# Kernel tuning notes

Hardware: AMD Instinct MI355X
Metric: run time of the kernel (lower is better)

The kernel has to match this reference:

```python
import jax, jax.numpy as jnp
import numpy as np

B, N, H, NH = 2, 2048, 1024, 16
D = H // NH  # head_dim = 64


def setup_inputs() -> dict:
    key = jax.random.key(0)
    ks = jax.random.split(key, 12)
    s = 0.02
    inp = {
        'q': jax.random.normal(ks[0], (B, N, H), jnp.float32),
        'k': jax.random.normal(ks[1], (B, N, H), jnp.float32),
        'v': jax.random.normal(ks[2], (B, N, H), jnp.float32),
        # causal mask: 1 where attending allowed, 0 above diagonal
        'mask': jnp.tril(jnp.ones((N, N), jnp.float32))[None, None],
        'Wq': jax.random.normal(ks[3], (H, H), jnp.float32) * s,
        'bq': jnp.zeros((H,), jnp.float32),
        'Wk': jax.random.normal(ks[4], (H, H), jnp.float32) * s,
        'bk': jnp.zeros((H,), jnp.float32),
        'Wv': jax.random.normal(ks[5], (H, H), jnp.float32) * s,
        'bv': jnp.zeros((H,), jnp.float32),
        'Wp': jax.random.normal(ks[6], (H, H), jnp.float32) * s,
        'bp': jnp.zeros((H,), jnp.float32),
    }
    return inp


def _split_heads(x):
    # [b, n, (h d)] -> [b, h, n, d]
    b, n, _ = x.shape
    return x.reshape(b, n, NH, D).transpose(0, 2, 1, 3)


def reference(q, k, v, mask, Wq, bq, Wk, bk, Wv, bv, Wp, bp):
    # torch nn.Linear: x @ W.T + b
    Q = _split_heads(q @ Wq.T + bq)                      # [b, h, n, d]
    K = _split_heads(k @ Wk.T + bk)
    V = _split_heads(v @ Wv.T + bv)
    scores = jnp.einsum('bhnd,bhmd->bhnm', Q, K) / jnp.sqrt(jnp.float32(D))
    scores = jnp.where(mask == 0, -jnp.inf, scores)      # masked_fill
    attn = jax.nn.softmax(scores, axis=-1)
    out = jnp.einsum('bhnm,bhmd->bhnd', attn, V)         # [b, h, n, d]
    out = out.transpose(0, 2, 1, 3).reshape(q.shape[0], q.shape[1], H)
    # dropout is identity in eval mode
    return out @ Wp.T + bp
```

## Files before the change

kernel.cpp:

```cpp
#include <hip/hip_runtime.h>

typedef unsigned short u16;
typedef __attribute__((ext_vector_type(8))) short bf16x8;
typedef __attribute__((ext_vector_type(4))) short bf16x4;
typedef __attribute__((ext_vector_type(4))) float f32x4;

#define NB 2
#define SEQ 2048
#define HID 1024
#define NHEAD 16
#define HD 64
#define MROWS (NB * SEQ)

__device__ __forceinline__ float bf2f(u16 u) {
  union { unsigned u; float f; } x; x.u = ((unsigned)u) << 16; return x.f;
}
__device__ __forceinline__ u16 f2bf(float f) {
  union { float f; unsigned u; } x; x.f = f;
  unsigned r = x.u + 0x7fffu + ((x.u >> 16) & 1u);
  return (u16)(r >> 16);
}
__device__ __forceinline__ u16 f2bf_trunc(float f) {
  union { float f; unsigned u; } x; x.f = f;
  return (u16)(x.u >> 16);
}

#define GLOAD_LDS16(g, l)                                                   \
  __builtin_amdgcn_global_load_lds(                                         \
      (const __attribute__((address_space(1))) void*)(g),                   \
      (__attribute__((address_space(3))) void*)(l), 16, 0, 0)

__global__ __launch_bounds__(256)
void conv_all(const float* __restrict__ q, const float* __restrict__ k,
              const float* __restrict__ v, const float* __restrict__ wq,
              const float* __restrict__ wk, const float* __restrict__ wv,
              const float* __restrict__ wp, u16* __restrict__ qb,
              u16* __restrict__ kb, u16* __restrict__ vb,
              u16* __restrict__ wcat, u16* __restrict__ wpb)
{
  const int i = blockIdx.x * 256 + threadIdx.x;
  const float* s; u16* d;
  if (i < 1572864) {
    const int seg = i / 524288;
    const int off = i - seg * 524288;
    s = (seg == 0 ? q : seg == 1 ? k : v) + (size_t)off * 8;
    d = (seg == 0 ? qb : seg == 1 ? kb : vb) + (size_t)off * 8;
  } else {
    const int j = i - 1572864;
    const int seg = j / 131072;
    const int off = j - seg * 131072;
    s = (seg == 0 ? wq : seg == 1 ? wk : seg == 2 ? wv : wp) + (size_t)off * 8;
    d = (seg < 3 ? wcat + (size_t)seg * 1048576 : wpb) + (size_t)off * 8;
  }
  f32x4 a = *(const f32x4*)s;
  f32x4 b = *(const f32x4*)(s + 4);
  bf16x8 o;
#pragma unroll
  for (int j = 0; j < 4; ++j) { o[j] = (short)f2bf(a[j]); o[4 + j] = (short)f2bf(b[j]); }
  *(bf16x8*)d = o;
}

__global__ __launch_bounds__(256)
void gemm_qkv(const u16* __restrict__ A0, const u16* __restrict__ A1,
              const u16* __restrict__ A2, const u16* __restrict__ Wcat,
              const float* __restrict__ b0, const float* __restrict__ b1,
              const float* __restrict__ b2,
              u16* __restrict__ Qh, u16* __restrict__ Kh, u16* __restrict__ Vt,
              float qscale)
{
  __shared__ u16 As[2 * 128 * 64];
  __shared__ u16 Bs[2 * 128 * 64];
  const int p = blockIdx.x;
  const int c = p & 7;
  const int i_ = p >> 3;
  const int G = c * 12 + (i_ % 12);
  const int j = i_ / 12;
  const int g = G >> 5;
  const int m0 = (G & 31) * 128;
  const int n0 = (g * 8 + j) * 128;
  const u16* A = (g == 0) ? A0 : (g == 1) ? A1 : A2;
  const float* bias = (g == 0) ? b0 : (g == 1) ? b1 : b2;
  const int t = threadIdx.x, lane = t & 63, w = t >> 6;
  const int grp = lane >> 4, lr = lane & 15;
  const int wr = (w >> 1) * 64, wc = (w & 1) * 64;
  const int sw8 = lr & 7;

  f32x4 acc[4][4];
#pragma unroll
  for (int i = 0; i < 4; ++i)
#pragma unroll
    for (int j2 = 0; j2 < 4; ++j2) acc[i][j2] = (f32x4){0.f, 0.f, 0.f, 0.f};

  const int srow8 = lane >> 3;
  const int achunk = ((lane & 7) ^ srow8) * 8;
  const u16* ag = A + (size_t)(m0 + w * 32 + srow8) * HID + achunk;
  const u16* wg = Wcat + (size_t)(n0 + w * 32 + srow8) * HID + achunk;

#define STAGE(BI, K0)                                                \
  {                                                                  \
    const u16* ab = ag + (K0);                                       \
    const u16* wb = wg + (K0);                                       \
    u16* al = As + (BI) * 8192 + (w * 32) * 64;                      \
    u16* bl = Bs + (BI) * 8192 + (w * 32) * 64;                      \
    GLOAD_LDS16(ab, al);                                             \
    GLOAD_LDS16(ab + (size_t)8 * HID, al + 8 * 64);                  \
    GLOAD_LDS16(ab + (size_t)16 * HID, al + 16 * 64);                \
    GLOAD_LDS16(ab + (size_t)24 * HID, al + 24 * 64);                \
    GLOAD_LDS16(wb, bl);                                             \
    GLOAD_LDS16(wb + (size_t)8 * HID, bl + 8 * 64);                  \
    GLOAD_LDS16(wb + (size_t)16 * HID, bl + 16 * 64);                \
    GLOAD_LDS16(wb + (size_t)24 * HID, bl + 24 * 64);                \
  }

  STAGE(0, 0);

  for (int it = 0; it < 16; ++it) {
    const int cur = it & 1;
    asm volatile("s_waitcnt vmcnt(0)" ::: "memory");
    __builtin_amdgcn_s_barrier();
    __builtin_amdgcn_sched_barrier(0);
    asm volatile("" ::: "memory");
    if (it < 15) STAGE(cur ^ 1, (it + 1) * 64);
    const u16* Ab = As + cur * 8192;
    const u16* Bb = Bs + cur * 8192;
#pragma unroll
    for (int kh = 0; kh < 2; ++kh) {
      bf16x8 af[4], bf[4];
#pragma unroll
      for (int mi = 0; mi < 4; ++mi)
        af[mi] = *(const bf16x8*)&Ab[(wr + mi * 16 + lr) * 64 +
                                     (((kh * 4 + grp) ^ sw8) * 8)];
#pragma unroll
      for (int ni = 0; ni < 4; ++ni)
        bf[ni] = *(const bf16x8*)&Bb[(wc + ni * 16 + lr) * 64 +
                                     (((kh * 4 + grp) ^ sw8) * 8)];
      __builtin_amdgcn_s_setprio(1);
#pragma unroll
      for (int mi = 0; mi < 4; ++mi)
#pragma unroll
        for (int ni = 0; ni < 4; ++ni)
          acc[mi][ni] = __builtin_amdgcn_mfma_f32_16x16x32_bf16(
              af[mi], bf[ni], acc[mi][ni], 0, 0, 0);
      __builtin_amdgcn_s_setprio(0);
    }
  }
#undef STAGE

  const float scale = (g == 0) ? qscale : 1.f;
#pragma unroll
  for (int mi = 0; mi < 4; ++mi) {
#pragma unroll
    for (int ni = 0; ni < 4; ++ni) {
      const int nl = (n0 & (HID - 1)) + wc + ni * 16 + lr;
      const float bval = bias[nl];
      const int mb = m0 + wr + mi * 16 + grp * 4;
      const int h = nl >> 6, d = nl & (HD - 1);
      if (g == 2) {
        const int b = mb >> 11, nn = mb & (SEQ - 1);
        bf16x4 pk;
#pragma unroll
        for (int r = 0; r < 4; ++r)
          pk[r] = (short)f2bf(acc[mi][ni][r] + bval);
        *(bf16x4*)&Vt[((size_t)(b * NHEAD + h) * HD + d) * SEQ + nn] = pk;
      } else {
        u16* O = (g == 0) ? Qh : Kh;
#pragma unroll
        for (int r = 0; r < 4; ++r) {
          const int m = mb + r;
          const int b = m >> 11, nn = m & (SEQ - 1);
          O[((size_t)(b * NHEAD + h) * SEQ + nn) * HD + d] =
              f2bf((acc[mi][ni][r] + bval) * scale);
        }
      }
    }
  }
}

__global__ __launch_bounds__(256)
void gemm_proj(const u16* __restrict__ A, const u16* __restrict__ W,
               const float* __restrict__ bias, float* __restrict__ Op)
{
  __shared__ u16 As[2 * 128 * 64];
  __shared__ u16 Bs[2 * 128 * 64];
  const int p = blockIdx.x;
  const int c = p & 7;
  const int i_ = p >> 3;
  const int G = c * 4 + (i_ & 3);
  const int j = i_ >> 2;
  const int m0 = G * 128, n0 = j * 128;
  const int t = threadIdx.x, lane = t & 63, w = t >> 6;
  const int grp = lane >> 4, lr = lane & 15;
  const int wr = (w >> 1) * 64, wc = (w & 1) * 64;
  const int sw8 = lr & 7;

  f32x4 acc[4][4];
#pragma unroll
  for (int i = 0; i < 4; ++i)
#pragma unroll
    for (int j2 = 0; j2 < 4; ++j2) acc[i][j2] = (f32x4){0.f, 0.f, 0.f, 0.f};

  const int srow8 = lane >> 3;
  const int achunk = ((lane & 7) ^ srow8) * 8;
  const u16* ag = A + (size_t)(m0 + w * 32 + srow8) * HID + achunk;
  const u16* wg = W + (size_t)(n0 + w * 32 + srow8) * HID + achunk;

#define STAGE(BI, K0)                                                \
  {                                                                  \
    const u16* ab = ag + (K0);                                       \
    const u16* wb = wg + (K0);                                       \
    u16* al = As + (BI) * 8192 + (w * 32) * 64;                      \
    u16* bl = Bs + (BI) * 8192 + (w * 32) * 64;                      \
    GLOAD_LDS16(ab, al);                                             \
    GLOAD_LDS16(ab + (size_t)8 * HID, al + 8 * 64);                  \
    GLOAD_LDS16(ab + (size_t)16 * HID, al + 16 * 64);                \
    GLOAD_LDS16(ab + (size_t)24 * HID, al + 24 * 64);                \
    GLOAD_LDS16(wb, bl);                                             \
    GLOAD_LDS16(wb + (size_t)8 * HID, bl + 8 * 64);                  \
    GLOAD_LDS16(wb + (size_t)16 * HID, bl + 16 * 64);                \
    GLOAD_LDS16(wb + (size_t)24 * HID, bl + 24 * 64);                \
  }

  STAGE(0, 0);

  for (int it = 0; it < 16; ++it) {
    const int cur = it & 1;
    asm volatile("s_waitcnt vmcnt(0)" ::: "memory");
    __builtin_amdgcn_s_barrier();
    __builtin_amdgcn_sched_barrier(0);
    asm volatile("" ::: "memory");
    if (it < 15) STAGE(cur ^ 1, (it + 1) * 64);
    const u16* Ab = As + cur * 8192;
    const u16* Bb = Bs + cur * 8192;
#pragma unroll
    for (int kh = 0; kh < 2; ++kh) {
      bf16x8 af[4], bf[4];
#pragma unroll
      for (int mi = 0; mi < 4; ++mi)
        af[mi] = *(const bf16x8*)&Ab[(wr + mi * 16 + lr) * 64 +
                                     (((kh * 4 + grp) ^ sw8) * 8)];
#pragma unroll
      for (int ni = 0; ni < 4; ++ni)
        bf[ni] = *(const bf16x8*)&Bb[(wc + ni * 16 + lr) * 64 +
                                     (((kh * 4 + grp) ^ sw8) * 8)];
      __builtin_amdgcn_s_setprio(1);
#pragma unroll
      for (int mi = 0; mi < 4; ++mi)
#pragma unroll
        for (int ni = 0; ni < 4; ++ni)
          acc[mi][ni] = __builtin_amdgcn_mfma_f32_16x16x32_bf16(
              af[mi], bf[ni], acc[mi][ni], 0, 0, 0);
      __builtin_amdgcn_s_setprio(0);
    }
  }
#undef STAGE

#pragma unroll
  for (int mi = 0; mi < 4; ++mi) {
#pragma unroll
    for (int ni = 0; ni < 4; ++ni) {
      const int n = n0 + wc + ni * 16 + lr;
      const float bval = bias[n];
      const int mb = m0 + wr + mi * 16 + grp * 4;
#pragma unroll
      for (int r = 0; r < 4; ++r)
        Op[(size_t)(mb + r) * HID + n] = acc[mi][ni][r] + bval;
    }
  }
}

__global__ __launch_bounds__(512)
void attn_fwd(const u16* __restrict__ Q, const u16* __restrict__ K,
              const u16* __restrict__ Vt, u16* __restrict__ parO,
              float* __restrict__ parL)
{
  __shared__ u16 KB[2][4096];
  __shared__ u16 VB[2][4096];
  const int bh = blockIdx.y;
  const int t = threadIdx.x;
  const int w = t >> 6, lane = t & 63;
  const int grp = lane >> 4, lr = lane & 15;
  const int px = blockIdx.x;
  const int parity = px & 1;
  const int qtA = px >> 1;
  const int qtB = 15 - qtA;
  const int q0A = qtA * 128 + w * 16;
  const int q0B = qtB * 128 + w * 16;
  const int ntB = 2 * qtB + 2;
  const size_t base = (size_t)bh * SEQ * HD;
  const float NEGINF = -__builtin_inff();

  const int srow = lane >> 3;
  const int scol = (lane & 7) ^ srow;
  const u16* kg = K + base + (size_t)(w * 8 + srow) * HD + scol * 8;
  const u16* vg = Vt + base + (size_t)(w * 8 + srow) * SEQ + scol * 8;

  const bf16x8 aqA0 = *(const bf16x8*)&Q[base + (size_t)(q0A + lr) * HD + grp * 8];
  const bf16x8 aqA1 = *(const bf16x8*)&Q[base + (size_t)(q0A + lr) * HD + grp * 8 + 32];
  const bf16x8 aqB0 = *(const bf16x8*)&Q[base + (size_t)(q0B + lr) * HD + grp * 8];
  const bf16x8 aqB1 = *(const bf16x8*)&Q[base + (size_t)(q0B + lr) * HD + grp * 8 + 32];

  float lA = 0.f, lB = 0.f;
  f32x4 oA[4], oB[4];
#pragma unroll
  for (int c = 0; c < 4; ++c) {
    oA[c] = (f32x4){0.f, 0.f, 0.f, 0.f};
    oB[c] = (f32x4){0.f, 0.f, 0.f, 0.f};
  }

  const int idqA = q0A >> 6;
  const int idqB = q0B >> 6;
  const int sw = lr & 7;

#define STAGE(bi, j0)                                              \
  {                                                                \
    GLOAD_LDS16(kg + (size_t)(j0) * HD, &KB[bi][w * 512]);         \
    GLOAD_LDS16(vg + (j0), &VB[bi][w * 512]);                      \
  }

#define COMPUTE(Q0, AQ0, AQ1, OACC, LI, IDQ)                                  \
  do {                                                                        \
    f32x4 sv[4];                                                              \
    __builtin_amdgcn_s_setprio(1);                                            \
    _Pragma("unroll")                                                         \
    for (int st = 0; st < 4; ++st) {                                          \
      const int ro = (st * 16 + lr) * 64;                                     \
      bf16x8 k0 = *(const bf16x8*)&KB[bi][ro + ((grp ^ sw) * 8)];             \
      bf16x8 k1 = *(const bf16x8*)&KB[bi][ro + (((grp + 4) ^ sw) * 8)];       \
      f32x4 s = (f32x4){0.f, 0.f, 0.f, 0.f};                                  \
      s = __builtin_amdgcn_mfma_f32_16x16x32_bf16(k0, (AQ0), s, 0, 0, 0);     \
      s = __builtin_amdgcn_mfma_f32_16x16x32_bf16(k1, (AQ1), s, 0, 0, 0);     \
      sv[st] = s;                                                             \
    }                                                                         \
    __builtin_amdgcn_s_setprio(0);                                            \
    bf16x4 bv[4][4];                                                          \
    _Pragma("unroll")                                                         \
    for (int st = 0; st < 4; ++st)                                            \
      _Pragma("unroll")                                                       \
      for (int c = 0; c < 4; ++c)                                             \
        bv[st][c] = *(const bf16x4*)&VB[bi][(c * 16 + lr) * 64 +              \
                        (((st * 2 + (grp >> 1)) ^ sw) * 8) + (grp & 1) * 4];  \
    if (it == (IDQ)) {                                                        \
      const int j0 = it << 6, qg = (Q0) + lr;                                 \
      _Pragma("unroll")                                                       \
      for (int st = 0; st < 4; ++st)                                          \
        _Pragma("unroll")                                                     \
        for (int r = 0; r < 4; ++r)                                           \
          if (j0 + st * 16 + grp * 4 + r > qg) sv[st][r] = NEGINF;            \
    }                                                                         \
    float rs = 0.f;                                                           \
    _Pragma("unroll")                                                         \
    for (int st = 0; st < 4; ++st)                                            \
      _Pragma("unroll")                                                       \
      for (int r = 0; r < 4; ++r) {                                           \
        sv[st][r] = exp2f(sv[st][r]);                                         \
        rs += sv[st][r];                                                      \
      }                                                                       \
    (LI) += rs;                                                               \
    bf16x4 pa[4];                                                             \
    _Pragma("unroll")                                                         \
    for (int st = 0; st < 4; ++st)                                            \
      _Pragma("unroll")                                                       \
      for (int r = 0; r < 4; ++r) pa[st][r] = (short)f2bf_trunc(sv[st][r]);   \
    __builtin_amdgcn_s_setprio(1);                                            \
    _Pragma("unroll")                                                         \
    for (int st = 0; st < 4; ++st)                                            \
      _Pragma("unroll")                                                       \
      for (int c = 0; c < 4; ++c)                                             \
        (OACC)[c] = __builtin_amdgcn_mfma_f32_16x16x16bf16_1k(                \
            pa[st], bv[st][c], (OACC)[c], 0, 0, 0);                           \
    __builtin_amdgcn_s_setprio(0);                                            \
  } while (0)

  STAGE(0, parity << 6);

  for (int it = parity; it < ntB; it += 2) {
    const int bi = ((it - parity) >> 1) & 1;
    asm volatile("s_waitcnt vmcnt(0)" ::: "memory");
    __builtin_amdgcn_s_barrier();
    __builtin_amdgcn_sched_barrier(0);
    asm volatile("" ::: "memory");
    if (it + 2 < ntB) STAGE(bi ^ 1, (it + 2) << 6);

    if (it <= idqB) COMPUTE(q0B, aqB0, aqB1, oB, lB, idqB);
    if (it <= idqA) COMPUTE(q0A, aqA0, aqA1, oA, lA, idqA);
  }
#undef STAGE
#undef COMPUTE

  lB += __shfl_xor(lB, 16);  lB += __shfl_xor(lB, 32);
  lA += __shfl_xor(lA, 16);  lA += __shfl_xor(lA, 32);

  const size_t pbase = (size_t)(parity * 32 + bh) * SEQ;
  if (grp == 0) {
    parL[pbase + q0B + lr] = lB;
    parL[pbase + q0A + lr] = lA;
  }
#pragma unroll
  for (int r = 0; r < 4; ++r) {
    const int nB = q0B + grp * 4 + r;
    const int nA = q0A + grp * 4 + r;
#pragma unroll
    for (int c = 0; c < 4; ++c) {
      parO[(pbase + nB) * HD + c * 16 + lr] = f2bf(oB[c][r]);
      parO[(pbase + nA) * HD + c * 16 + lr] = f2bf(oA[c][r]);
    }
  }
}

__global__ __launch_bounds__(256)
void combine(const u16* __restrict__ parO, const float* __restrict__ parL,
             u16* __restrict__ AO)
{
  const int i = blockIdx.x * 256 + threadIdx.x;
  const int bh = i >> 14;
  const int rem = i & 16383;
  const int n = rem >> 3;
  const int d0 = (rem & 7) * 8;
  const size_t q0 = (size_t)bh * SEQ + n;
  const float inv = 1.f / (parL[q0] + parL[q0 + 65536]);
  const u16* p0 = parO + q0 * HD + d0;
  const u16* p1 = p0 + (size_t)4194304;
  bf16x8 a = *(const bf16x8*)p0;
  bf16x8 b = *(const bf16x8*)p1;
  bf16x8 o;
#pragma unroll
  for (int j = 0; j < 8; ++j)
    o[j] = (short)f2bf((bf2f((u16)a[j]) + bf2f((u16)b[j])) * inv);
  const int bb = bh >> 4, h = bh & 15;
  *(bf16x8*)&AO[((size_t)(bb * SEQ + n)) * HID + h * HD + d0] = o;
}

extern "C" void kernel_launch(void* const* d_in, const int* in_sizes, int n_in,
                              void* d_out, int out_size, void* d_ws, size_t ws_size,
                              hipStream_t stream) {
  const float* q  = (const float*)d_in[0];
  const float* k  = (const float*)d_in[1];
  const float* v  = (const float*)d_in[2];
  const float* Wq = (const float*)d_in[4];
  const float* bq = (const float*)d_in[5];
  const float* Wk = (const float*)d_in[6];
  const float* bk = (const float*)d_in[7];
  const float* Wv = (const float*)d_in[8];
  const float* bv = (const float*)d_in[9];
  const float* Wp = (const float*)d_in[10];
  const float* bp = (const float*)d_in[11];
  float* out = (float*)d_out;

  char* ws = (char*)d_ws;
  u16*   qb   = (u16*)(ws);
  u16*   kb   = (u16*)(ws + ( 8u << 20));
  u16*   vb   = (u16*)(ws + (16u << 20));
  u16*   Wcat = (u16*)(ws + (24u << 20));
  u16*   Wpb  = (u16*)(ws + (30u << 20));
  u16*   Qh   = (u16*)(ws + (32u << 20));
  u16*   Kh   = (u16*)(ws + (40u << 20));
  u16*   Vt   = (u16*)(ws + (48u << 20));
  u16*   parO = (u16*)(ws);
  float* parL = (float*)(ws + (17u << 20));
  u16*   AO   = (u16*)(ws + (18u << 20));

  const float qscale = 0.125f * 1.4426950408889634f;

  conv_all<<<8192, 256, 0, stream>>>(q, k, v, Wq, Wk, Wv, Wp,
                                     qb, kb, vb, Wcat, Wpb);
  gemm_qkv<<<768, 256, 0, stream>>>(
      qb, kb, vb, Wcat, bq, bk, bv, Qh, Kh, Vt, qscale);
  attn_fwd<<<dim3(16, NB * NHEAD), 512, 0, stream>>>(Qh, Kh, Vt, parO, parL);
  combine<<<2048, 256, 0, stream>>>(parO, parL, AO);
  gemm_proj<<<256, 256, 0, stream>>>(AO, Wpb, bp, out);
}
```

Measured before the change: 123.6 us.

## Fuse input bf16 conversion into QKV GEMM and split-combine into projection GEMM

The QKV GEMM now loads fp32 activations directly, converts them to bf16 in registers and writes them into swizzled LDS, so the separate activation conversion pass and its bf16 round trip through memory go away. The projection GEMM likewise reads the two partial attention outputs and their normalisers, combines them on the fly and stages the result into LDS, which removes the combine kernel and the AO buffer. Both GEMMs move to 128x64 tiles with twice as many blocks to keep parallelism up. The cost is that every N-tile block rereads and reconverts the same A rows (fp32 for QKV, two bf16 partials for projection), and the register-staged A path adds conversion work and manual vmcnt pipelining inside the main loop.

```diff
diff --git a/kernel.cpp b/kernel.cpp
--- a/kernel.cpp
+++ b/kernel.cpp
@@ -31,27 +31,16 @@
       (__attribute__((address_space(3))) void*)(l), 16, 0, 0)
 
 __global__ __launch_bounds__(256)
-void conv_all(const float* __restrict__ q, const float* __restrict__ k,
-              const float* __restrict__ v, const float* __restrict__ wq,
-              const float* __restrict__ wk, const float* __restrict__ wv,
-              const float* __restrict__ wp, u16* __restrict__ qb,
-              u16* __restrict__ kb, u16* __restrict__ vb,
-              u16* __restrict__ wcat, u16* __restrict__ wpb)
+void conv_w(const float* __restrict__ wq, const float* __restrict__ wk,
+            const float* __restrict__ wv, const float* __restrict__ wp,
+            u16* __restrict__ wcat, u16* __restrict__ wpb)
 {
   const int i = blockIdx.x * 256 + threadIdx.x;
-  const float* s; u16* d;
-  if (i < 1572864) {
-    const int seg = i / 524288;
-    const int off = i - seg * 524288;
-    s = (seg == 0 ? q : seg == 1 ? k : v) + (size_t)off * 8;
-    d = (seg == 0 ? qb : seg == 1 ? kb : vb) + (size_t)off * 8;
-  } else {
-    const int j = i - 1572864;
-    const int seg = j / 131072;
-    const int off = j - seg * 131072;
-    s = (seg == 0 ? wq : seg == 1 ? wk : seg == 2 ? wv : wp) + (size_t)off * 8;
-    d = (seg < 3 ? wcat + (size_t)seg * 1048576 : wpb) + (size_t)off * 8;
-  }
+  const int seg = i >> 17;
+  const int off = i & 131071;
+  const float* s = (seg == 0 ? wq : seg == 1 ? wk : seg == 2 ? wv : wp) +
+                   (size_t)off * 8;
+  u16* d = (seg < 3 ? wcat + (size_t)seg * 1048576 : wpb) + (size_t)off * 8;
   f32x4 a = *(const f32x4*)s;
   f32x4 b = *(const f32x4*)(s + 4);
   bf16x8 o;
@@ -61,97 +50,119 @@
 }
 
 __global__ __launch_bounds__(256)
-void gemm_qkv(const u16* __restrict__ A0, const u16* __restrict__ A1,
-              const u16* __restrict__ A2, const u16* __restrict__ Wcat,
+void gemm_qkv(const float* __restrict__ A0, const float* __restrict__ A1,
+              const float* __restrict__ A2, const u16* __restrict__ Wcat,
               const float* __restrict__ b0, const float* __restrict__ b1,
               const float* __restrict__ b2,
               u16* __restrict__ Qh, u16* __restrict__ Kh, u16* __restrict__ Vt,
               float qscale)
 {
   __shared__ u16 As[2 * 128 * 64];
-  __shared__ u16 Bs[2 * 128 * 64];
+  __shared__ u16 Bs[2 * 64 * 64];
   const int p = blockIdx.x;
-  const int c = p & 7;
+  const int cx = p & 7;
   const int i_ = p >> 3;
-  const int G = c * 12 + (i_ % 12);
-  const int j = i_ / 12;
+  const int G = cx * 12 + (i_ >> 4);
+  const int j = i_ & 15;
   const int g = G >> 5;
   const int m0 = (G & 31) * 128;
-  const int n0 = (g * 8 + j) * 128;
-  const u16* A = (g == 0) ? A0 : (g == 1) ? A1 : A2;
+  const int nloc0 = j * 64;
+  const float* A = (g == 0) ? A0 : (g == 1) ? A1 : A2;
   const float* bias = (g == 0) ? b0 : (g == 1) ? b1 : b2;
   const int t = threadIdx.x, lane = t & 63, w = t >> 6;
   const int grp = lane >> 4, lr = lane & 15;
-  const int wr = (w >> 1) * 64, wc = (w & 1) * 64;
+  const int wr = (w >> 1) * 64, wc = (w & 1) * 32;
   const int sw8 = lr & 7;
 
-  f32x4 acc[4][4];
+  f32x4 acc[4][2];
 #pragma unroll
   for (int i = 0; i < 4; ++i)
 #pragma unroll
-    for (int j2 = 0; j2 < 4; ++j2) acc[i][j2] = (f32x4){0.f, 0.f, 0.f, 0.f};
+    for (int j2 = 0; j2 < 2; ++j2) acc[i][j2] = (f32x4){0.f, 0.f, 0.f, 0.f};
 
   const int srow8 = lane >> 3;
   const int achunk = ((lane & 7) ^ srow8) * 8;
-  const u16* ag = A + (size_t)(m0 + w * 32 + srow8) * HID + achunk;
-  const u16* wg = Wcat + (size_t)(n0 + w * 32 + srow8) * HID + achunk;
-
-#define STAGE(BI, K0)                                                \
-  {                                                                  \
-    const u16* ab = ag + (K0);                                       \
-    const u16* wb = wg + (K0);                                       \
-    u16* al = As + (BI) * 8192 + (w * 32) * 64;                      \
-    u16* bl = Bs + (BI) * 8192 + (w * 32) * 64;                      \
-    GLOAD_LDS16(ab, al);                                             \
-    GLOAD_LDS16(ab + (size_t)8 * HID, al + 8 * 64);                  \
-    GLOAD_LDS16(ab + (size_t)16 * HID, al + 16 * 64);                \
-    GLOAD_LDS16(ab + (size_t)24 * HID, al + 24 * 64);                \
-    GLOAD_LDS16(wb, bl);                                             \
-    GLOAD_LDS16(wb + (size_t)8 * HID, bl + 8 * 64);                  \
-    GLOAD_LDS16(wb + (size_t)16 * HID, bl + 16 * 64);                \
-    GLOAD_LDS16(wb + (size_t)24 * HID, bl + 24 * 64);                \
-  }
-
-  STAGE(0, 0);
+  const u16* wg = Wcat + (size_t)(g * 1024 + nloc0 + w * 16 + srow8) * HID + achunk;
+  const int r = t >> 1, kh2 = t & 1;
+  const float* ag = A + (size_t)(m0 + r) * HID + kh2 * 32;
+  const int wbase = r * 64 + 0;
+
+  f32x4 a4[8];
+#define ALOADQ(K0)                                                    \
+  { const float* pp = ag + (K0);                                      \
+    a4[0] = *(const f32x4*)(pp);      a4[1] = *(const f32x4*)(pp + 4);  \
+    a4[2] = *(const f32x4*)(pp + 8);  a4[3] = *(const f32x4*)(pp + 12); \
+    a4[4] = *(const f32x4*)(pp + 16); a4[5] = *(const f32x4*)(pp + 20); \
+    a4[6] = *(const f32x4*)(pp + 24); a4[7] = *(const f32x4*)(pp + 28); }
+#define ACONVQ(BI)                                                    \
+  { _Pragma("unroll")                                                 \
+    for (int jj = 0; jj < 4; ++jj) {                                  \
+      bf16x8 o;                                                       \
+      _Pragma("unroll")                                               \
+      for (int e = 0; e < 4; ++e) {                                   \
+        o[e]     = (short)f2bf(a4[2 * jj][e]);                        \
+        o[4 + e] = (short)f2bf(a4[2 * jj + 1][e]);                    \
+      }                                                               \
+      const int q = kh2 * 4 + jj;                                     \
+      *(bf16x8*)&As[(BI) * 8192 + wbase + ((q ^ (r & 7)) * 8)] = o;   \
+    } }
+#define WSTAGEQ(BI, K0)                                               \
+  { const u16* wb = wg + (K0);                                        \
+    u16* bl = Bs + (BI) * 4096 + (w * 16) * 64;                       \
+    GLOAD_LDS16(wb, bl);                                              \
+    GLOAD_LDS16(wb + (size_t)8 * HID, bl + 8 * 64); }
+
+  ALOADQ(0);
+  asm volatile("s_waitcnt vmcnt(0)" ::: "memory");
+  ACONVQ(0);
+  WSTAGEQ(0, 0);
+  ALOADQ(64);
+  asm volatile("s_waitcnt lgkmcnt(0)" ::: "memory");
 
   for (int it = 0; it < 16; ++it) {
     const int cur = it & 1;
-    asm volatile("s_waitcnt vmcnt(0)" ::: "memory");
+    asm volatile("s_waitcnt vmcnt(8)" ::: "memory");
     __builtin_amdgcn_s_barrier();
     __builtin_amdgcn_sched_barrier(0);
     asm volatile("" ::: "memory");
-    if (it < 15) STAGE(cur ^ 1, (it + 1) * 64);
+    WSTAGEQ(cur ^ 1, (it + 1 < 16) ? (it + 1) * 64 : 0);
     const u16* Ab = As + cur * 8192;
-    const u16* Bb = Bs + cur * 8192;
+    const u16* Bb = Bs + cur * 4096;
 #pragma unroll
     for (int kh = 0; kh < 2; ++kh) {
-      bf16x8 af[4], bf[4];
+      bf16x8 af[4], bf[2];
 #pragma unroll
       for (int mi = 0; mi < 4; ++mi)
         af[mi] = *(const bf16x8*)&Ab[(wr + mi * 16 + lr) * 64 +
                                      (((kh * 4 + grp) ^ sw8) * 8)];
 #pragma unroll
-      for (int ni = 0; ni < 4; ++ni)
+      for (int ni = 0; ni < 2; ++ni)
         bf[ni] = *(const bf16x8*)&Bb[(wc + ni * 16 + lr) * 64 +
                                      (((kh * 4 + grp) ^ sw8) * 8)];
       __builtin_amdgcn_s_setprio(1);
 #pragma unroll
       for (int mi = 0; mi < 4; ++mi)
 #pragma unroll
-        for (int ni = 0; ni < 4; ++ni)
+        for (int ni = 0; ni < 2; ++ni)
           acc[mi][ni] = __builtin_amdgcn_mfma_f32_16x16x32_bf16(
               af[mi], bf[ni], acc[mi][ni], 0, 0, 0);
       __builtin_amdgcn_s_setprio(0);
     }
-  }
-#undef STAGE
+    asm volatile("s_waitcnt vmcnt(2)" ::: "memory");
+    ACONVQ(cur ^ 1);
+    ALOADQ((it + 2 < 16) ? (it + 2) * 64 : 0);
+    asm volatile("s_waitcnt lgkmcnt(0)" ::: "memory");
+  }
+#undef ALOADQ
+#undef ACONVQ
+#undef WSTAGEQ
 
   const float scale = (g == 0) ? qscale : 1.f;
 #pragma unroll
   for (int mi = 0; mi < 4; ++mi) {
 #pragma unroll
-    for (int ni = 0; ni < 4; ++ni) {
-      const int nl = (n0 & (HID - 1)) + wc + ni * 16 + lr;
+    for (int ni = 0; ni < 2; ++ni) {
+      const int nl = nloc0 + wc + ni * 16 + lr;
       const float bval = bias[nl];
       const int mb = m0 + wr + mi * 16 + grp * 4;
       const int h = nl >> 6, d = nl & (HD - 1);
@@ -159,17 +170,17 @@
         const int b = mb >> 11, nn = mb & (SEQ - 1);
         bf16x4 pk;
 #pragma unroll
-        for (int r = 0; r < 4; ++r)
-          pk[r] = (short)f2bf(acc[mi][ni][r] + bval);
+        for (int rr = 0; rr < 4; ++rr)
+          pk[rr] = (short)f2bf(acc[mi][ni][rr] + bval);
         *(bf16x4*)&Vt[((size_t)(b * NHEAD + h) * HD + d) * SEQ + nn] = pk;
       } else {
         u16* O = (g == 0) ? Qh : Kh;
 #pragma unroll
-        for (int r = 0; r < 4; ++r) {
-          const int m = mb + r;
+        for (int rr = 0; rr < 4; ++rr) {
+          const int m = mb + rr;
           const int b = m >> 11, nn = m & (SEQ - 1);
           O[((size_t)(b * NHEAD + h) * SEQ + nn) * HD + d] =
-              f2bf((acc[mi][ni][r] + bval) * scale);
+              f2bf((acc[mi][ni][rr] + bval) * scale);
         }
       }
     }
@@ -177,93 +188,124 @@
 }
 
 __global__ __launch_bounds__(256)
-void gemm_proj(const u16* __restrict__ A, const u16* __restrict__ W,
-               const float* __restrict__ bias, float* __restrict__ Op)
+void gemm_proj(const u16* __restrict__ parO, const float* __restrict__ parL,
+               const u16* __restrict__ W, const float* __restrict__ bias,
+               float* __restrict__ Op)
 {
   __shared__ u16 As[2 * 128 * 64];
-  __shared__ u16 Bs[2 * 128 * 64];
+  __shared__ u16 Bs[2 * 64 * 64];
   const int p = blockIdx.x;
-  const int c = p & 7;
+  const int cx = p & 7;
   const int i_ = p >> 3;
-  const int G = c * 4 + (i_ & 3);
+  const int G = cx * 4 + (i_ & 3);
   const int j = i_ >> 2;
-  const int m0 = G * 128, n0 = j * 128;
+  const int m0 = G * 128, n0 = j * 64;
   const int t = threadIdx.x, lane = t & 63, w = t >> 6;
   const int grp = lane >> 4, lr = lane & 15;
-  const int wr = (w >> 1) * 64, wc = (w & 1) * 64;
+  const int wr = (w >> 1) * 64, wc = (w & 1) * 32;
   const int sw8 = lr & 7;
 
-  f32x4 acc[4][4];
+  f32x4 acc[4][2];
 #pragma unroll
   for (int i = 0; i < 4; ++i)
 #pragma unroll
-    for (int j2 = 0; j2 < 4; ++j2) acc[i][j2] = (f32x4){0.f, 0.f, 0.f, 0.f};
+    for (int j2 = 0; j2 < 2; ++j2) acc[i][j2] = (f32x4){0.f, 0.f, 0.f, 0.f};
 
   const int srow8 = lane >> 3;
   const int achunk = ((lane & 7) ^ srow8) * 8;
-  const u16* ag = A + (size_t)(m0 + w * 32 + srow8) * HID + achunk;
-  const u16* wg = W + (size_t)(n0 + w * 32 + srow8) * HID + achunk;
-
-#define STAGE(BI, K0)                                                \
-  {                                                                  \
-    const u16* ab = ag + (K0);                                       \
-    const u16* wb = wg + (K0);                                       \
-    u16* al = As + (BI) * 8192 + (w * 32) * 64;                      \
-    u16* bl = Bs + (BI) * 8192 + (w * 32) * 64;                      \
-    GLOAD_LDS16(ab, al);                                             \
-    GLOAD_LDS16(ab + (size_t)8 * HID, al + 8 * 64);                  \
-    GLOAD_LDS16(ab + (size_t)16 * HID, al + 16 * 64);                \
-    GLOAD_LDS16(ab + (size_t)24 * HID, al + 24 * 64);                \
-    GLOAD_LDS16(wb, bl);                                             \
-    GLOAD_LDS16(wb + (size_t)8 * HID, bl + 8 * 64);                  \
-    GLOAD_LDS16(wb + (size_t)16 * HID, bl + 16 * 64);                \
-    GLOAD_LDS16(wb + (size_t)24 * HID, bl + 24 * 64);                \
-  }
-
-  STAGE(0, 0);
+  const u16* wg = W + (size_t)(n0 + w * 16 + srow8) * HID + achunk;
+  const int r = t >> 1, dh = t & 1;
+  const int m = m0 + r;
+  const int b = m >> 11, nn = m & (SEQ - 1);
+  const u16* po0 = parO + ((size_t)(b * NHEAD) * SEQ + nn) * HD + dh * 32;
+  const u16* po1 = po0 + (size_t)32 * SEQ * HD;
+  const float* pl0 = parL + (size_t)(b * NHEAD) * SEQ + nn;
+  const int wbase = r * 64;
+
+  bf16x8 av[8];
+  float l0, l1;
+#define ALOADP(H)                                                     \
+  { const u16* q0 = po0 + (size_t)(H) * (SEQ * HD);                   \
+    const u16* q1 = po1 + (size_t)(H) * (SEQ * HD);                   \
+    av[0] = *(const bf16x8*)(q0);      av[1] = *(const bf16x8*)(q0 + 8);  \
+    av[2] = *(const bf16x8*)(q0 + 16); av[3] = *(const bf16x8*)(q0 + 24); \
+    av[4] = *(const bf16x8*)(q1);      av[5] = *(const bf16x8*)(q1 + 8);  \
+    av[6] = *(const bf16x8*)(q1 + 16); av[7] = *(const bf16x8*)(q1 + 24); \
+    l0 = pl0[(size_t)(H) * SEQ];                                      \
+    l1 = pl0[(size_t)(H) * SEQ + 32 * SEQ]; }
+#define ACONVP(BI)                                                    \
+  { const float inv = 1.f / (l0 + l1);                                \
+    _Pragma("unroll")                                                 \
+    for (int jj = 0; jj < 4; ++jj) {                                  \
+      bf16x8 o;                                                       \
+      _Pragma("unroll")                                               \
+      for (int e = 0; e < 8; ++e)                                     \
+        o[e] = (short)f2bf((bf2f((u16)av[jj][e]) +                    \
+                            bf2f((u16)av[4 + jj][e])) * inv);         \
+      const int q = dh * 4 + jj;                                      \
+      *(bf16x8*)&As[(BI) * 8192 + wbase + ((q ^ (r & 7)) * 8)] = o;   \
+    } }
+#define WSTAGEP(BI, K0)                                               \
+  { const u16* wb = wg + (K0);                                        \
+    u16* bl = Bs + (BI) * 4096 + (w * 16) * 64;                       \
+    GLOAD_LDS16(wb, bl);                                              \
+    GLOAD_LDS16(wb + (size_t)8 * HID, bl + 8 * 64); }
+
+  ALOADP(0);
+  asm volatile("s_waitcnt vmcnt(0)" ::: "memory");
+  ACONVP(0);
+  WSTAGEP(0, 0);
+  ALOADP(1);
+  asm volatile("s_waitcnt lgkmcnt(0)" ::: "memory");
 
   for (int it = 0; it < 16; ++it) {
     const int cur = it & 1;
-    asm volatile("s_waitcnt vmcnt(0)" ::: "memory");
+    asm volatile("s_waitcnt vmcnt(10)" ::: "memory");
     __builtin_amdgcn_s_barrier();
     __builtin_amdgcn_sched_barrier(0);
     asm volatile("" ::: "memory");
-    if (it < 15) STAGE(cur ^ 1, (it + 1) * 64);
+    WSTAGEP(cur ^ 1, (it + 1 < 16) ? (it + 1) * 64 : 0);
     const u16* Ab = As + cur * 8192;
-    const u16* Bb = Bs + cur * 8192;
+    const u16* Bb = Bs + cur * 4096;
 #pragma unroll
     for (int kh = 0; kh < 2; ++kh) {
-      bf16x8 af[4], bf[4];
+      bf16x8 af[4], bf[2];
 #pragma unroll
       for (int mi = 0; mi < 4; ++mi)
         af[mi] = *(const bf16x8*)&Ab[(wr + mi * 16 + lr) * 64 +
                                      (((kh * 4 + grp) ^ sw8) * 8)];
 #pragma unroll
-      for (int ni = 0; ni < 4; ++ni)
+      for (int ni = 0; ni < 2; ++ni)
         bf[ni] = *(const bf16x8*)&Bb[(wc + ni * 16 + lr) * 64 +
                                      (((kh * 4 + grp) ^ sw8) * 8)];
       __builtin_amdgcn_s_setprio(1);
 #pragma unroll
       for (int mi = 0; mi < 4; ++mi)
 #pragma unroll
-        for (int ni = 0; ni < 4; ++ni)
+        for (int ni = 0; ni < 2; ++ni)
           acc[mi][ni] = __builtin_amdgcn_mfma_f32_16x16x32_bf16(
               af[mi], bf[ni], acc[mi][ni], 0, 0, 0);
       __builtin_amdgcn_s_setprio(0);
     }
-  }
-#undef STAGE
+    asm volatile("s_waitcnt vmcnt(2)" ::: "memory");
+    ACONVP(cur ^ 1);
+    ALOADP((it + 2 < 16) ? (it + 2) : 0);
+    asm volatile("s_waitcnt lgkmcnt(0)" ::: "memory");
+  }
+#undef ALOADP
+#undef ACONVP
+#undef WSTAGEP
 
 #pragma unroll
   for (int mi = 0; mi < 4; ++mi) {
 #pragma unroll
-    for (int ni = 0; ni < 4; ++ni) {
+    for (int ni = 0; ni < 2; ++ni) {
       const int n = n0 + wc + ni * 16 + lr;
       const float bval = bias[n];
       const int mb = m0 + wr + mi * 16 + grp * 4;
 #pragma unroll
-      for (int r = 0; r < 4; ++r)
-        Op[(size_t)(mb + r) * HID + n] = acc[mi][ni][r] + bval;
+      for (int rr = 0; rr < 4; ++rr)
+        Op[(size_t)(mb + rr) * HID + n] = acc[mi][ni][rr] + bval;
     }
   }
 }
@@ -407,29 +449,6 @@
   }
 }
 
-__global__ __launch_bounds__(256)
-void combine(const u16* __restrict__ parO, const float* __restrict__ parL,
-             u16* __restrict__ AO)
-{
-  const int i = blockIdx.x * 256 + threadIdx.x;
-  const int bh = i >> 14;
-  const int rem = i & 16383;
-  const int n = rem >> 3;
-  const int d0 = (rem & 7) * 8;
-  const size_t q0 = (size_t)bh * SEQ + n;
-  const float inv = 1.f / (parL[q0] + parL[q0 + 65536]);
-  const u16* p0 = parO + q0 * HD + d0;
-  const u16* p1 = p0 + (size_t)4194304;
-  bf16x8 a = *(const bf16x8*)p0;
-  bf16x8 b = *(const bf16x8*)p1;
-  bf16x8 o;
-#pragma unroll
-  for (int j = 0; j < 8; ++j)
-    o[j] = (short)f2bf((bf2f((u16)a[j]) + bf2f((u16)b[j])) * inv);
-  const int bb = bh >> 4, h = bh & 15;
-  *(bf16x8*)&AO[((size_t)(bb * SEQ + n)) * HID + h * HD + d0] = o;
-}
-
 extern "C" void kernel_launch(void* const* d_in, const int* in_sizes, int n_in,
                               void* d_out, int out_size, void* d_ws, size_t ws_size,
                               hipStream_t stream) {
@@ -447,25 +466,19 @@
   float* out = (float*)d_out;
 
   char* ws = (char*)d_ws;
-  u16*   qb   = (u16*)(ws);
-  u16*   kb   = (u16*)(ws + ( 8u << 20));
-  u16*   vb   = (u16*)(ws + (16u << 20));
+  u16*   parO = (u16*)(ws);
+  float* parL = (float*)(ws + (17u << 20));
   u16*   Wcat = (u16*)(ws + (24u << 20));
   u16*   Wpb  = (u16*)(ws + (30u << 20));
   u16*   Qh   = (u16*)(ws + (32u << 20));
   u16*   Kh   = (u16*)(ws + (40u << 20));
   u16*   Vt   = (u16*)(ws + (48u << 20));
-  u16*   parO = (u16*)(ws);
-  float* parL = (float*)(ws + (17u << 20));
-  u16*   AO   = (u16*)(ws + (18u << 20));
 
   const float qscale = 0.125f * 1.4426950408889634f;
 
-  conv_all<<<8192, 256, 0, stream>>>(q, k, v, Wq, Wk, Wv, Wp,
-                                     qb, kb, vb, Wcat, Wpb);
-  gemm_qkv<<<768, 256, 0, stream>>>(
-      qb, kb, vb, Wcat, bq, bk, bv, Qh, Kh, Vt, qscale);
+  conv_w<<<2048, 256, 0, stream>>>(Wq, Wk, Wv, Wp, Wcat, Wpb);
+  gemm_qkv<<<1536, 256, 0, stream>>>(
+      q, k, v, Wcat, bq, bk, bv, Qh, Kh, Vt, qscale);
   attn_fwd<<<dim3(16, NB * NHEAD), 512, 0, stream>>>(Qh, Kh, Vt, parO, parL);
-  combine<<<2048, 256, 0, stream>>>(parO, parL, AO);
-  gemm_proj<<<256, 256, 0, stream>>>(AO, Wpb, bp, out);
-}
+  gemm_proj<<<512, 256, 0, stream>>>(parO, parL, Wpb, bp, out);
+}
```

Result: slower. 183.9 us (+48.8%).

## Fuse split-KV combine into output projection GEMM A-operand staging

Applied to the files above, without the earlier changes.

Removes the separate combine kernel by having gemm_proj read the two partial attention outputs and their row sums directly, normalise them in registers, and write the bf16 A tile into LDS. The N tile is halved to 64 so the grid doubles to 512 blocks, giving better CU fill. A-operand loads now go through registers with manual vmcnt bookkeeping instead of direct-to-LDS loads. The cost is that each partial output is re-read and re-normalised once per N tile (16 times instead of once), and the correctness of the pipelining depends on hand-counted waitcnt values.

```diff
diff --git a/kernel.cpp b/kernel.cpp
--- a/kernel.cpp
+++ b/kernel.cpp
@@ -177,93 +177,124 @@
 }
 
 __global__ __launch_bounds__(256)
-void gemm_proj(const u16* __restrict__ A, const u16* __restrict__ W,
-               const float* __restrict__ bias, float* __restrict__ Op)
+void gemm_proj(const u16* __restrict__ parO, const float* __restrict__ parL,
+               const u16* __restrict__ W, const float* __restrict__ bias,
+               float* __restrict__ Op)
 {
   __shared__ u16 As[2 * 128 * 64];
-  __shared__ u16 Bs[2 * 128 * 64];
+  __shared__ u16 Bs[2 * 64 * 64];
   const int p = blockIdx.x;
-  const int c = p & 7;
+  const int cx = p & 7;
   const int i_ = p >> 3;
-  const int G = c * 4 + (i_ & 3);
+  const int G = cx * 4 + (i_ & 3);
   const int j = i_ >> 2;
-  const int m0 = G * 128, n0 = j * 128;
+  const int m0 = G * 128, n0 = j * 64;
   const int t = threadIdx.x, lane = t & 63, w = t >> 6;
   const int grp = lane >> 4, lr = lane & 15;
-  const int wr = (w >> 1) * 64, wc = (w & 1) * 64;
+  const int wr = (w >> 1) * 64, wc = (w & 1) * 32;
   const int sw8 = lr & 7;
 
-  f32x4 acc[4][4];
+  f32x4 acc[4][2];
 #pragma unroll
   for (int i = 0; i < 4; ++i)
 #pragma unroll
-    for (int j2 = 0; j2 < 4; ++j2) acc[i][j2] = (f32x4){0.f, 0.f, 0.f, 0.f};
+    for (int j2 = 0; j2 < 2; ++j2) acc[i][j2] = (f32x4){0.f, 0.f, 0.f, 0.f};
 
   const int srow8 = lane >> 3;
   const int achunk = ((lane & 7) ^ srow8) * 8;
-  const u16* ag = A + (size_t)(m0 + w * 32 + srow8) * HID + achunk;
-  const u16* wg = W + (size_t)(n0 + w * 32 + srow8) * HID + achunk;
-
-#define STAGE(BI, K0)                                                \
-  {                                                                  \
-    const u16* ab = ag + (K0);                                       \
-    const u16* wb = wg + (K0);                                       \
-    u16* al = As + (BI) * 8192 + (w * 32) * 64;                      \
-    u16* bl = Bs + (BI) * 8192 + (w * 32) * 64;                      \
-    GLOAD_LDS16(ab, al);                                             \
-    GLOAD_LDS16(ab + (size_t)8 * HID, al + 8 * 64);                  \
-    GLOAD_LDS16(ab + (size_t)16 * HID, al + 16 * 64);                \
-    GLOAD_LDS16(ab + (size_t)24 * HID, al + 24 * 64);                \
-    GLOAD_LDS16(wb, bl);                                             \
-    GLOAD_LDS16(wb + (size_t)8 * HID, bl + 8 * 64);                  \
-    GLOAD_LDS16(wb + (size_t)16 * HID, bl + 16 * 64);                \
-    GLOAD_LDS16(wb + (size_t)24 * HID, bl + 24 * 64);                \
-  }
-
-  STAGE(0, 0);
+  const u16* wg = W + (size_t)(n0 + w * 16 + srow8) * HID + achunk;
+  const int r = t >> 1, dh = t & 1;
+  const int m = m0 + r;
+  const int b = m >> 11, nn = m & (SEQ - 1);
+  const u16* po0 = parO + ((size_t)(b * NHEAD) * SEQ + nn) * HD + dh * 32;
+  const u16* po1 = po0 + (size_t)32 * SEQ * HD;
+  const float* pl0 = parL + (size_t)(b * NHEAD) * SEQ + nn;
+  const int wbase = r * 64;
+
+  bf16x8 av[8];
+  float l0, l1;
+#define ALOADP(H)                                                     \
+  { const u16* q0 = po0 + (size_t)(H) * (SEQ * HD);                   \
+    const u16* q1 = po1 + (size_t)(H) * (SEQ * HD);                   \
+    av[0] = *(const bf16x8*)(q0);      av[1] = *(const bf16x8*)(q0 + 8);  \
+    av[2] = *(const bf16x8*)(q0 + 16); av[3] = *(const bf16x8*)(q0 + 24); \
+    av[4] = *(const bf16x8*)(q1);      av[5] = *(const bf16x8*)(q1 + 8);  \
+    av[6] = *(const bf16x8*)(q1 + 16); av[7] = *(const bf16x8*)(q1 + 24); \
+    l0 = pl0[(size_t)(H) * SEQ];                                      \
+    l1 = pl0[(size_t)(H) * SEQ + 32 * SEQ]; }
+#define ACONVP(BI)                                                    \
+  { const float inv = 1.f / (l0 + l1);                                \
+    _Pragma("unroll")                                                 \
+    for (int jj = 0; jj < 4; ++jj) {                                  \
+      bf16x8 o;                                                       \
+      _Pragma("unroll")                                               \
+      for (int e = 0; e < 8; ++e)                                     \
+        o[e] = (short)f2bf((bf2f((u16)av[jj][e]) +                    \
+                            bf2f((u16)av[4 + jj][e])) * inv);         \
+      const int q = dh * 4 + jj;                                      \
+      *(bf16x8*)&As[(BI) * 8192 + wbase + ((q ^ (r & 7)) * 8)] = o;   \
+    } }
+#define WSTAGEP(BI, K0)                                               \
+  { const u16* wb = wg + (K0);                                        \
+    u16* bl = Bs + (BI) * 4096 + (w * 16) * 64;                       \
+    GLOAD_LDS16(wb, bl);                                              \
+    GLOAD_LDS16(wb + (size_t)8 * HID, bl + 8 * 64); }
+
+  ALOADP(0);
+  asm volatile("s_waitcnt vmcnt(0)" ::: "memory");
+  ACONVP(0);
+  WSTAGEP(0, 0);
+  ALOADP(1);
+  asm volatile("s_waitcnt lgkmcnt(0)" ::: "memory");
 
   for (int it = 0; it < 16; ++it) {
     const int cur = it & 1;
-    asm volatile("s_waitcnt vmcnt(0)" ::: "memory");
+    asm volatile("s_waitcnt vmcnt(10)" ::: "memory");
     __builtin_amdgcn_s_barrier();
     __builtin_amdgcn_sched_barrier(0);
     asm volatile("" ::: "memory");
-    if (it < 15) STAGE(cur ^ 1, (it + 1) * 64);
+    WSTAGEP(cur ^ 1, (it + 1 < 16) ? (it + 1) * 64 : 0);
     const u16* Ab = As + cur * 8192;
-    const u16* Bb = Bs + cur * 8192;
+    const u16* Bb = Bs + cur * 4096;
 #pragma unroll
     for (int kh = 0; kh < 2; ++kh) {
-      bf16x8 af[4], bf[4];
+      bf16x8 af[4], bf[2];
 #pragma unroll
       for (int mi = 0; mi < 4; ++mi)
         af[mi] = *(const bf16x8*)&Ab[(wr + mi * 16 + lr) * 64 +
                                      (((kh * 4 + grp) ^ sw8) * 8)];
 #pragma unroll
-      for (int ni = 0; ni < 4; ++ni)
+      for (int ni = 0; ni < 2; ++ni)
         bf[ni] = *(const bf16x8*)&Bb[(wc + ni * 16 + lr) * 64 +
                                      (((kh * 4 + grp) ^ sw8) * 8)];
       __builtin_amdgcn_s_setprio(1);
 #pragma unroll
       for (int mi = 0; mi < 4; ++mi)
 #pragma unroll
-        for (int ni = 0; ni < 4; ++ni)
+        for (int ni = 0; ni < 2; ++ni)
           acc[mi][ni] = __builtin_amdgcn_mfma_f32_16x16x32_bf16(
               af[mi], bf[ni], acc[mi][ni], 0, 0, 0);
       __builtin_amdgcn_s_setprio(0);
     }
-  }
-#undef STAGE
+    asm volatile("s_waitcnt vmcnt(2)" ::: "memory");
+    ACONVP(cur ^ 1);
+    ALOADP((it + 2 < 16) ? (it + 2) : 0);
+    asm volatile("s_waitcnt lgkmcnt(0)" ::: "memory");
+  }
+#undef ALOADP
+#undef ACONVP
+#undef WSTAGEP
 
 #pragma unroll
   for (int mi = 0; mi < 4; ++mi) {
 #pragma unroll
-    for (int ni = 0; ni < 4; ++ni) {
+    for (int ni = 0; ni < 2; ++ni) {
       const int n = n0 + wc + ni * 16 + lr;
       const float bval = bias[n];
       const int mb = m0 + wr + mi * 16 + grp * 4;
 #pragma unroll
-      for (int r = 0; r < 4; ++r)
-        Op[(size_t)(mb + r) * HID + n] = acc[mi][ni][r] + bval;
+      for (int rr = 0; rr < 4; ++rr)
+        Op[(size_t)(mb + rr) * HID + n] = acc[mi][ni][rr] + bval;
     }
   }
 }
@@ -407,29 +438,6 @@
   }
 }
 
-__global__ __launch_bounds__(256)
-void combine(const u16* __restrict__ parO, const float* __restrict__ parL,
-             u16* __restrict__ AO)
-{
-  const int i = blockIdx.x * 256 + threadIdx.x;
-  const int bh = i >> 14;
-  const int rem = i & 16383;
-  const int n = rem >> 3;
-  const int d0 = (rem & 7) * 8;
-  const size_t q0 = (size_t)bh * SEQ + n;
-  const float inv = 1.f / (parL[q0] + parL[q0 + 65536]);
-  const u16* p0 = parO + q0 * HD + d0;
-  const u16* p1 = p0 + (size_t)4194304;
-  bf16x8 a = *(const bf16x8*)p0;
-  bf16x8 b = *(const bf16x8*)p1;
-  bf16x8 o;
-#pragma unroll
-  for (int j = 0; j < 8; ++j)
-    o[j] = (short)f2bf((bf2f((u16)a[j]) + bf2f((u16)b[j])) * inv);
-  const int bb = bh >> 4, h = bh & 15;
-  *(bf16x8*)&AO[((size_t)(bb * SEQ + n)) * HID + h * HD + d0] = o;
-}
-
 extern "C" void kernel_launch(void* const* d_in, const int* in_sizes, int n_in,
                               void* d_out, int out_size, void* d_ws, size_t ws_size,
                               hipStream_t stream) {
@@ -457,7 +465,6 @@
   u16*   Vt   = (u16*)(ws + (48u << 20));
   u16*   parO = (u16*)(ws);
   float* parL = (float*)(ws + (17u << 20));
-  u16*   AO   = (u16*)(ws + (18u << 20));
 
   const float qscale = 0.125f * 1.4426950408889634f;
 
@@ -466,6 +473,5 @@
   gemm_qkv<<<768, 256, 0, stream>>>(
       qb, kb, vb, Wcat, bq, bk, bv, Qh, Kh, Vt, qscale);
   attn_fwd<<<dim3(16, NB * NHEAD), 512, 0, stream>>>(Qh, Kh, Vt, parO, parL);
-  combine<<<2048, 256, 0, stream>>>(parO, parL, AO);
-  gemm_proj<<<256, 256, 0, stream>>>(AO, Wpb, bp, out);
-}
+  gemm_proj<<<512, 256, 0, stream>>>(parO, parL, Wpb, bp, out);
+}
```

Measured after the change: 127.1 us. +2.8%, slower.
